# Kernel optimization log

Measured on AMD Instinct MI355X. Metric: run time of the kernel, lower is better.

Reference implementation:

```python
import jax, jax.numpy as jnp
import numpy as np

E = 64          # num_experts
DIM = 1024      # model dim
HID = 512       # per-expert FFN hidden dim
N = 65536       # total routed tokens (1024 per expert)


def setup_inputs() -> dict:
    key = jax.random.key(0)
    k_x, k1, k2, k3 = jax.random.split(key, 4)
    x = jax.random.normal(k_x, (N, DIM), dtype=jnp.float32)
    # learned params: w1/w3 [E, HID, DIM], w2 [E, DIM, HID] (trunc_normal std 0.02 ~ normal*0.02)
    w1 = jax.random.normal(k1, (E, HID, DIM), dtype=jnp.float32) * 0.02
    w2 = jax.random.normal(k2, (E, DIM, HID), dtype=jnp.float32) * 0.02
    w3 = jax.random.normal(k3, (E, HID, DIM), dtype=jnp.float32) * 0.02
    num_tokens_per_expert = jnp.full((E,), N // E, dtype=jnp.int32)
    return {"x": x, "w1": w1, "w2": w2, "w3": w3,
            "num_tokens_per_expert": num_tokens_per_expert}


def reference(x, w1, w2, w3, num_tokens_per_expert):
    # Grouped-GEMM SwiGLU expert FFN (torch._grouped_mm path, bf16 compute).
    bf16 = jnp.bfloat16
    xb = x.astype(bf16)                                   # [N, DIM]
    g = num_tokens_per_expert                             # [E] int32 group sizes
    w1t = jnp.swapaxes(w1.astype(bf16), 1, 2)             # [E, DIM, HID]
    w3t = jnp.swapaxes(w3.astype(bf16), 1, 2)             # [E, DIM, HID]
    w2t = jnp.swapaxes(w2.astype(bf16), 1, 2)             # [E, HID, DIM]
    h = jax.nn.silu(jax.lax.ragged_dot(xb, w1t, g))       # [N, HID]
    h = h * jax.lax.ragged_dot(xb, w3t, g)                # fused gate
    out = jax.lax.ragged_dot(h, w2t, g)                   # [N, DIM]
    return out.astype(x.dtype)
```

## Files before the change

kernel.cpp:

```cpp
#include <hip/hip_runtime.h>
#include <hip/hip_bf16.h>
#include <stdint.h>

#define NE   64
#define DIM  1024
#define HID  512
#define TPE  1024

typedef __attribute__((ext_vector_type(8)))  __bf16          bf16x8;
typedef __attribute__((ext_vector_type(4)))  float           f32x4;
typedef __attribute__((ext_vector_type(8)))  unsigned short  ushort8_t;
typedef __attribute__((ext_vector_type(4)))  float           float4_t;

__device__ __forceinline__ unsigned short f2bf(float f) {
  return __builtin_bit_cast(unsigned short, static_cast<__bf16>(f));
}
__device__ __forceinline__ float bf2f(unsigned short u) {
  unsigned int x = ((unsigned int)u) << 16;
  return __builtin_bit_cast(float, x);
}
__device__ __forceinline__ ushort8_t pack8(float4_t a, float4_t b) {
  ushort8_t r;
  r[0] = f2bf(a[0]); r[1] = f2bf(a[1]); r[2] = f2bf(a[2]); r[3] = f2bf(a[3]);
  r[4] = f2bf(b[0]); r[5] = f2bf(b[1]); r[6] = f2bf(b[2]); r[7] = f2bf(b[3]);
  return r;
}
__device__ __forceinline__ bf16x8 ldsfrag(const unsigned short* p) {
  return __builtin_bit_cast(bf16x8, *reinterpret_cast<const ushort8_t*>(p));
}

__device__ __forceinline__ void barrier_lgkm() {
  asm volatile("s_waitcnt lgkmcnt(0)" ::: "memory");
  __builtin_amdgcn_s_barrier();
}

#define LDK 40

__device__ __forceinline__ int xcd_swizzle(int bid, int nwg) {
  return (bid & 7) * (nwg >> 3) + (bid >> 3);
}

#define P1_NKT (DIM / 32)

__global__ __launch_bounds__(256, 2) void p1_kernel(
    const float* __restrict__ X, const float* __restrict__ W1,
    const float* __restrict__ W3, unsigned short* __restrict__ H) {
  __shared__ __align__(16) unsigned short lA [2][256 * LDK];
  __shared__ __align__(16) unsigned short lB1[2][ 64 * LDK];
  __shared__ __align__(16) unsigned short lB3[2][ 64 * LDK];

  const int tile = xcd_swizzle(blockIdx.x, NE * 4 * 8);
  const int e  = tile >> 5;
  const int tn = (tile >> 2) & 7;
  const int tm = tile & 3;
  const int t  = threadIdx.x;

  const float* gA  = X  + (size_t)(e * TPE + tm * 256) * DIM;
  const float* gB1 = W1 + ((size_t)e * HID + tn * 64) * DIM;
  const float* gB3 = W3 + ((size_t)e * HID + tn * 64) * DIM;

  const int ar = t >> 2, ac = (t & 3) * 8;

  float4_t a0[4][2], b10[2], b30[2];
  float4_t a1[4][2], b11[2], b31[2];

  auto load_g = [&](float4_t (&a)[4][2], float4_t (&b1)[2], float4_t (&b3)[2],
                    int kt) {
#pragma unroll
    for (int i = 0; i < 4; ++i) {
      const size_t o = (size_t)(ar + 64 * i) * DIM + kt * 32 + ac;
      a[i][0] = *reinterpret_cast<const float4_t*>(gA + o);
      a[i][1] = *reinterpret_cast<const float4_t*>(gA + o + 4);
    }
    const size_t ob = (size_t)ar * DIM + kt * 32 + ac;
    b1[0] = *reinterpret_cast<const float4_t*>(gB1 + ob);
    b1[1] = *reinterpret_cast<const float4_t*>(gB1 + ob + 4);
    b3[0] = *reinterpret_cast<const float4_t*>(gB3 + ob);
    b3[1] = *reinterpret_cast<const float4_t*>(gB3 + ob + 4);
  };
  auto store_l = [&](int buf, float4_t (&a)[4][2], float4_t (&b1)[2],
                     float4_t (&b3)[2]) {
#pragma unroll
    for (int i = 0; i < 4; ++i)
      *reinterpret_cast<ushort8_t*>(&lA[buf][(ar + 64 * i) * LDK + ac]) =
          pack8(a[i][0], a[i][1]);
    *reinterpret_cast<ushort8_t*>(&lB1[buf][ar * LDK + ac]) = pack8(b1[0], b1[1]);
    *reinterpret_cast<ushort8_t*>(&lB3[buf][ar * LDK + ac]) = pack8(b3[0], b3[1]);
  };

  const int lane = t & 63;
  const int wv   = t >> 6;
  const int wr   = wv >> 1, wc = wv & 1;
  const int fr   = lane & 15;
  const int ks   = (lane >> 4) * 8;

  f32x4 acc1[8][2], acc3[8][2];
#pragma unroll
  for (int m = 0; m < 8; ++m)
#pragma unroll
    for (int n = 0; n < 2; ++n)
#pragma unroll
      for (int i = 0; i < 4; ++i) { acc1[m][n][i] = 0.f; acc3[m][n][i] = 0.f; }

  auto mfma_phase = [&](int buf) {
    bf16x8 b1f[2], b3f[2];
#pragma unroll
    for (int n = 0; n < 2; ++n) {
      const int bi = (wc * 32 + n * 16 + fr) * LDK + ks;
      b1f[n] = ldsfrag(&lB1[buf][bi]);
      b3f[n] = ldsfrag(&lB3[buf][bi]);
    }
#pragma unroll
    for (int m = 0; m < 8; ++m) {
      const bf16x8 af = ldsfrag(&lA[buf][(wr * 128 + m * 16 + fr) * LDK + ks]);
#pragma unroll
      for (int n = 0; n < 2; ++n) {
        acc1[m][n] = __builtin_amdgcn_mfma_f32_16x16x32_bf16(af, b1f[n], acc1[m][n], 0, 0, 0);
        acc3[m][n] = __builtin_amdgcn_mfma_f32_16x16x32_bf16(af, b3f[n], acc3[m][n], 0, 0, 0);
      }
    }
  };

  load_g(a0, b10, b30, 0);
  load_g(a1, b11, b31, 1);
  for (int kt = 0; kt < P1_NKT; kt += 2) {
    store_l(0, a0, b10, b30);
    if (kt + 2 < P1_NKT) load_g(a0, b10, b30, kt + 2);
    barrier_lgkm();
    mfma_phase(0);
    store_l(1, a1, b11, b31);
    if (kt + 3 < P1_NKT) load_g(a1, b11, b31, kt + 3);
    barrier_lgkm();
    mfma_phase(1);
  }

  const int tokBase = e * TPE + tm * 256 + wr * 128 + (lane >> 4) * 4;
  const int hidBase = tn * 64 + wc * 32;
#pragma unroll
  for (int m = 0; m < 8; ++m)
#pragma unroll
    for (int n = 0; n < 2; ++n)
#pragma unroll
      for (int r = 0; r < 4; ++r) {
        const int tok = tokBase + m * 16 + r;
        const int hid = hidBase + n * 16 + fr;
        const float av = bf2f(f2bf(acc1[m][n][r]));
        const float bv = bf2f(f2bf(acc3[m][n][r]));
        const float s  = av / (1.0f + __expf(-av));
        H[(size_t)tok * HID + hid] = f2bf(s * bv);
      }
}

#define P2_NKT (HID / 32)

__global__ __launch_bounds__(256, 2) void p2_kernel(
    const unsigned short* __restrict__ Hin, const float* __restrict__ W2,
    float* __restrict__ OUT) {
  __shared__ __align__(16) unsigned short lA[2][256 * LDK];
  __shared__ __align__(16) unsigned short lB[2][128 * LDK];

  const int tile = xcd_swizzle(blockIdx.x, NE * 4 * 8);
  const int e  = tile >> 5;
  const int tn = (tile >> 2) & 7;
  const int tm = tile & 3;
  const int t  = threadIdx.x;

  const unsigned short* gA = Hin + (size_t)(e * TPE + tm * 256) * HID;
  const float*          gB = W2  + ((size_t)e * DIM + tn * 128) * HID;

  const int ar = t >> 2, ac = (t & 3) * 8;

  ushort8_t ha0[4], ha1[4];
  float4_t  wb0[2][2], wb1[2][2];

  auto load_g = [&](ushort8_t (&ha)[4], float4_t (&wb)[2][2], int kt) {
#pragma unroll
    for (int i = 0; i < 4; ++i)
      ha[i] = *reinterpret_cast<const ushort8_t*>(
          gA + (size_t)(ar + 64 * i) * HID + kt * 32 + ac);
#pragma unroll
    for (int i = 0; i < 2; ++i) {
      const size_t bo = (size_t)(ar + 64 * i) * HID + kt * 32 + ac;
      wb[i][0] = *reinterpret_cast<const float4_t*>(gB + bo);
      wb[i][1] = *reinterpret_cast<const float4_t*>(gB + bo + 4);
    }
  };
  auto store_l = [&](int buf, ushort8_t (&ha)[4], float4_t (&wb)[2][2]) {
#pragma unroll
    for (int i = 0; i < 4; ++i)
      *reinterpret_cast<ushort8_t*>(&lA[buf][(ar + 64 * i) * LDK + ac]) = ha[i];
#pragma unroll
    for (int i = 0; i < 2; ++i)
      *reinterpret_cast<ushort8_t*>(&lB[buf][(ar + 64 * i) * LDK + ac]) =
          pack8(wb[i][0], wb[i][1]);
  };

  const int lane = t & 63;
  const int wv   = t >> 6;
  const int wr   = wv >> 1, wc = wv & 1;
  const int fr   = lane & 15;
  const int ks   = (lane >> 4) * 8;

  f32x4 acc[8][4];
#pragma unroll
  for (int m = 0; m < 8; ++m)
#pragma unroll
    for (int n = 0; n < 4; ++n)
#pragma unroll
      for (int i = 0; i < 4; ++i) acc[m][n][i] = 0.f;

  auto mfma_phase = [&](int buf) {
    bf16x8 bfr[4];
#pragma unroll
    for (int n = 0; n < 4; ++n)
      bfr[n] = ldsfrag(&lB[buf][(wc * 64 + n * 16 + fr) * LDK + ks]);
#pragma unroll
    for (int m = 0; m < 8; ++m) {
      const bf16x8 af = ldsfrag(&lA[buf][(wr * 128 + m * 16 + fr) * LDK + ks]);
#pragma unroll
      for (int n = 0; n < 4; ++n)
        acc[m][n] = __builtin_amdgcn_mfma_f32_16x16x32_bf16(af, bfr[n], acc[m][n], 0, 0, 0);
    }
  };

  load_g(ha0, wb0, 0);
  load_g(ha1, wb1, 1);
  for (int kt = 0; kt < P2_NKT; kt += 2) {
    store_l(0, ha0, wb0);
    if (kt + 2 < P2_NKT) load_g(ha0, wb0, kt + 2);
    barrier_lgkm();
    mfma_phase(0);
    store_l(1, ha1, wb1);
    if (kt + 3 < P2_NKT) load_g(ha1, wb1, kt + 3);
    barrier_lgkm();
    mfma_phase(1);
  }

  const int tokBase = e * TPE + tm * 256 + wr * 128 + (lane >> 4) * 4;
  const int dBase   = tn * 128 + wc * 64;
#pragma unroll
  for (int m = 0; m < 8; ++m)
#pragma unroll
    for (int n = 0; n < 4; ++n)
#pragma unroll
      for (int r = 0; r < 4; ++r) {
        const int tok = tokBase + m * 16 + r;
        const int d   = dBase + n * 16 + fr;
        OUT[(size_t)tok * DIM + d] = bf2f(f2bf(acc[m][n][r]));
      }
}

extern "C" void kernel_launch(void* const* d_in, const int* in_sizes, int n_in,
                              void* d_out, int out_size, void* d_ws, size_t ws_size,
                              hipStream_t stream) {
  (void)in_sizes; (void)n_in; (void)out_size; (void)ws_size;
  const float* X  = (const float*)d_in[0];
  const float* W1 = (const float*)d_in[1];
  const float* W2 = (const float*)d_in[2];
  const float* W3 = (const float*)d_in[3];

  unsigned short* H = (unsigned short*)d_ws;
  float* OUT = (float*)d_out;

  p1_kernel<<<dim3(NE * 4 * 8), dim3(256), 0, stream>>>(X, W1, W3, H);
  p2_kernel<<<dim3(NE * 4 * 8), dim3(256), 0, stream>>>(H, W2, OUT);
}
```

Measured before the change: 517.5 us.

## Pre-convert weights to bf16 and rewrite GEMMs with direct global-to-LDS loads

Adds a weight-conversion kernel that casts W1/W3/W2 to bf16 once per call, interleaving W1 and W3 rows so one GEMM tile covers both gate and up projections. The two GEMM kernels are rewritten with 512-thread blocks, 256x256x64 tiles, XOR-swizzled LDS, and global_load_lds async copies for bf16 operands, with barriers and setprio placed around the MFMA blocks. The SwiGLU gate is combined through an LDS exchange between wave halves. This removes repeated fp32 weight loads and in-kernel conversion, at the cost of an extra pass over the weights and more workspace.

```diff
diff --git a/kernel.cpp b/kernel.cpp
--- a/kernel.cpp
+++ b/kernel.cpp
@@ -10,6 +10,7 @@
 typedef __attribute__((ext_vector_type(8)))  __bf16          bf16x8;
 typedef __attribute__((ext_vector_type(4)))  float           f32x4;
 typedef __attribute__((ext_vector_type(8)))  unsigned short  ushort8_t;
+typedef __attribute__((ext_vector_type(4)))  unsigned short  ushort4_t;
 typedef __attribute__((ext_vector_type(4)))  float           float4_t;
 
 __device__ __forceinline__ unsigned short f2bf(float f) {
@@ -28,226 +29,288 @@
 __device__ __forceinline__ bf16x8 ldsfrag(const unsigned short* p) {
   return __builtin_bit_cast(bf16x8, *reinterpret_cast<const ushort8_t*>(p));
 }
-
 __device__ __forceinline__ void barrier_lgkm() {
   asm volatile("s_waitcnt lgkmcnt(0)" ::: "memory");
   __builtin_amdgcn_s_barrier();
 }
-
-#define LDK 40
+typedef __attribute__((address_space(1))) const unsigned int gas_uint;
+typedef __attribute__((address_space(3))) unsigned int las_uint;
+__device__ __forceinline__ void gload16(const void* g, void* l) {
+  __builtin_amdgcn_global_load_lds((gas_uint*)g, (las_uint*)l, 16, 0, 0);
+}
 
 __device__ __forceinline__ int xcd_swizzle(int bid, int nwg) {
   return (bid & 7) * (nwg >> 3) + (bid >> 3);
 }
 
-#define P1_NKT (DIM / 32)
-
-__global__ __launch_bounds__(256, 2) void p1_kernel(
-    const float* __restrict__ X, const float* __restrict__ W1,
-    const float* __restrict__ W3, unsigned short* __restrict__ H) {
-  __shared__ __align__(16) unsigned short lA [2][256 * LDK];
-  __shared__ __align__(16) unsigned short lB1[2][ 64 * LDK];
-  __shared__ __align__(16) unsigned short lB3[2][ 64 * LDK];
-
-  const int tile = xcd_swizzle(blockIdx.x, NE * 4 * 8);
-  const int e  = tile >> 5;
-  const int tn = (tile >> 2) & 7;
+__global__ __launch_bounds__(256) void conv_w(
+    const float* __restrict__ W1, const float* __restrict__ W3,
+    const float* __restrict__ W2,
+    unsigned short* __restrict__ WB13, unsigned short* __restrict__ W2b) {
+  const int rb  = blockIdx.x;
+  const int reg = rb >> 9;
+  const int rbl = rb & 511;
+  const int f0  = rbl * 256 + threadIdx.x;
+  const int STRIDE = 512 * 256;
+
+  const float* src = (reg == 0) ? W1 : (reg == 1) ? W3 : W2;
+
+#pragma unroll 1
+  for (int it = 0; it < 8; ++it) {
+    float4_t v[4][2];
+    int f[4];
+#pragma unroll
+    for (int u = 0; u < 4; ++u) {
+      f[u] = f0 + (it * 4 + u) * STRIDE;
+      const float* p = src + (size_t)f[u] * 8;
+      v[u][0] = *reinterpret_cast<const float4_t*>(p);
+      v[u][1] = *reinterpret_cast<const float4_t*>(p + 4);
+    }
+#pragma unroll
+    for (int u = 0; u < 4; ++u) {
+      size_t dst;
+      if (reg == 2) {
+        dst = (size_t)f[u] * 8;
+        *reinterpret_cast<ushort8_t*>(W2b + dst) = pack8(v[u][0], v[u][1]);
+      } else {
+        const int e  = f[u] >> 16;
+        const int h  = (f[u] >> 7) & 511;
+        const int c8 = f[u] & 127;
+        const int g  = h >> 7, r = (h & 127) + (reg == 1 ? 128 : 0);
+        dst = ((((size_t)(e * 4 + g)) * 256 + r) * 128 + c8) * 8;
+        *reinterpret_cast<ushort8_t*>(WB13 + dst) = pack8(v[u][0], v[u][1]);
+      }
+    }
+  }
+}
+
+#define GEMM_IDS                                                               \
+  const int lane = threadIdx.x & 63;                                           \
+  const int wid  = threadIdx.x >> 6;                                           \
+  const int wr   = wid >> 2, wn = wid & 3;                                     \
+  const int fr   = lane & 15;                                                  \
+  const int c16b = lane >> 4;                                                  \
+  const int swz  = fr & 7;                                                     \
+  const int s_r  = lane >> 3;                                                  \
+  const int s_c  = ((lane & 7) ^ s_r) * 8;
+
+#define GEMM_ACC_INIT                                                          \
+  f32x4 acc[8][4];                                                             \
+  _Pragma("unroll") for (int m = 0; m < 8; ++m)                                \
+    _Pragma("unroll") for (int n = 0; n < 4; ++n)                              \
+      _Pragma("unroll") for (int i = 0; i < 4; ++i) acc[m][n][i] = 0.f;
+
+#define RD_FRAGS(buf, kk)                                                      \
+  bf16x8 af[8], bf0, bf1;                                                      \
+  (void)0
+
+__global__ __launch_bounds__(512, 2) void p1_fast(
+    const float* __restrict__ X, const unsigned short* __restrict__ WB13,
+    unsigned short* __restrict__ H) {
+  __shared__ __align__(16) unsigned short smem[2][2][256 * 64];
+
+  const int tile = xcd_swizzle(blockIdx.x, NE * 4 * 4);
+  const int e  = tile >> 4;
+  const int tm = (tile >> 2) & 3;
+  const int g  = tile & 3;
+  const float*          gA = X    + (size_t)(e * TPE + tm * 256) * DIM;
+  const unsigned short* gB = WB13 + (size_t)(e * 4 + g) * 256 * DIM;
+
+  GEMM_IDS
+  GEMM_ACC_INIT
+
+  const int arow = threadIdx.x >> 1, ah = threadIdx.x & 1;
+  float4_t fa[8];
+
+  auto loadA = [&](int kt) {
+    const float* p = gA + (size_t)arow * DIM + kt * 64 + ah * 32;
+#pragma unroll
+    for (int j = 0; j < 8; ++j)
+      fa[j] = *reinterpret_cast<const float4_t*>(p + j * 4);
+  };
+  auto writeA = [&](int buf) {
+    const int base = arow * 64;
+#pragma unroll
+    for (int j = 0; j < 4; ++j) {
+      const int gidx = (ah * 4 + j) ^ (arow & 7);
+      *reinterpret_cast<ushort8_t*>(&smem[buf][0][base + gidx * 8]) =
+          pack8(fa[2 * j], fa[2 * j + 1]);
+    }
+  };
+  auto stB = [&](int buf, int kt, int j) {
+    gload16(gB + (size_t)(j * 8 + s_r) * DIM + kt * 64 + s_c,
+            &smem[buf][1][j * 512]);
+  };
+  auto rdA = [&](int buf, int m, int kk) {
+    const int row = wr * 128 + m * 16 + fr;
+    return ldsfrag(&smem[buf][0][row * 64 + (((c16b + kk * 4) ^ swz) * 8)]);
+  };
+  auto rdB = [&](int buf, int nf, int kk) {
+    const int row = wn * 64 + nf * 16 + fr;
+    return ldsfrag(&smem[buf][1][row * 64 + (((c16b + kk * 4) ^ swz) * 8)]);
+  };
+
+  loadA(0);
+#pragma unroll 1
+  for (int j = 0; j < 4; ++j) stB(0, 0, wid * 4 + j);
+  writeA(0);
+
+  for (int kt = 0; kt < 16; ++kt) {
+    const int buf = kt & 1, sbuf = buf ^ 1;
+    const bool st = (kt + 1 < 16);
+    asm volatile("s_waitcnt vmcnt(0) lgkmcnt(0)" ::: "memory");
+    __builtin_amdgcn_s_barrier();
+    asm volatile("" ::: "memory");
+    if (st) loadA(kt + 1);
+    bf16x8 af[8];
+#pragma unroll
+    for (int q = 0; q < 4; ++q) {
+      const int kk = q >> 1, nh = q & 1;
+      if (nh == 0) {
+#pragma unroll
+        for (int m = 0; m < 8; ++m) af[m] = rdA(buf, m, kk);
+      }
+      bf16x8 bf0 = rdB(buf, nh * 2 + 0, kk);
+      bf16x8 bf1 = rdB(buf, nh * 2 + 1, kk);
+      if (st) stB(sbuf, kt + 1, wid * 4 + q);
+      asm volatile("" ::: "memory");
+      __builtin_amdgcn_s_barrier();
+      __builtin_amdgcn_s_setprio(1);
+#pragma unroll
+      for (int m = 0; m < 8; ++m) {
+        acc[m][nh * 2 + 0] = __builtin_amdgcn_mfma_f32_16x16x32_bf16(
+            af[m], bf0, acc[m][nh * 2 + 0], 0, 0, 0);
+        acc[m][nh * 2 + 1] = __builtin_amdgcn_mfma_f32_16x16x32_bf16(
+            af[m], bf1, acc[m][nh * 2 + 1], 0, 0, 0);
+      }
+      __builtin_amdgcn_s_setprio(0);
+    }
+    if (st) writeA(sbuf);
+  }
+
+  __builtin_amdgcn_s_barrier();
+  unsigned short* bex = &smem[0][0][0];
+  const int q4 = (lane >> 4) * 4;
+  if (wn >= 2) {
+#pragma unroll
+    for (int m = 0; m < 8; ++m)
+#pragma unroll
+      for (int n = 0; n < 4; ++n) {
+        const int hidl = (wn - 2) * 64 + n * 16 + fr;
+        const int tokl = wr * 128 + m * 16 + q4;
+        ushort4_t v;
+#pragma unroll
+        for (int r = 0; r < 4; ++r) v[r] = f2bf(acc[m][n][r]);
+        *reinterpret_cast<ushort4_t*>(&bex[hidl * 264 + tokl]) = v;
+      }
+  }
+  barrier_lgkm();
+  if (wn < 2) {
+    const int rowbase = e * TPE + tm * 256;
+#pragma unroll
+    for (int m = 0; m < 8; ++m)
+#pragma unroll
+      for (int n = 0; n < 4; ++n) {
+        const int hidl = wn * 64 + n * 16 + fr;
+        const int tokl = wr * 128 + m * 16 + q4;
+        const ushort4_t bv =
+            *reinterpret_cast<const ushort4_t*>(&bex[hidl * 264 + tokl]);
+#pragma unroll
+        for (int r = 0; r < 4; ++r) {
+          const float av = bf2f(f2bf(acc[m][n][r]));
+          const float b  = bf2f(bv[r]);
+          const float s  = av / (1.0f + __expf(-av));
+          H[(size_t)(rowbase + tokl + r) * HID + g * 128 + hidl] = f2bf(s * b);
+        }
+      }
+  }
+}
+
+__global__ __launch_bounds__(512, 2) void p2_fast(
+    const unsigned short* __restrict__ Hb, const unsigned short* __restrict__ W2b,
+    float* __restrict__ OUT) {
+  __shared__ __align__(16) unsigned short smem[2][2][256 * 64];
+
+  const int tile = xcd_swizzle(blockIdx.x, NE * 4 * 4);
+  const int e  = tile >> 4;
+  const int tn = (tile >> 2) & 3;
   const int tm = tile & 3;
-  const int t  = threadIdx.x;
-
-  const float* gA  = X  + (size_t)(e * TPE + tm * 256) * DIM;
-  const float* gB1 = W1 + ((size_t)e * HID + tn * 64) * DIM;
-  const float* gB3 = W3 + ((size_t)e * HID + tn * 64) * DIM;
-
-  const int ar = t >> 2, ac = (t & 3) * 8;
-
-  float4_t a0[4][2], b10[2], b30[2];
-  float4_t a1[4][2], b11[2], b31[2];
-
-  auto load_g = [&](float4_t (&a)[4][2], float4_t (&b1)[2], float4_t (&b3)[2],
-                    int kt) {
-#pragma unroll
-    for (int i = 0; i < 4; ++i) {
-      const size_t o = (size_t)(ar + 64 * i) * DIM + kt * 32 + ac;
-      a[i][0] = *reinterpret_cast<const float4_t*>(gA + o);
-      a[i][1] = *reinterpret_cast<const float4_t*>(gA + o + 4);
-    }
-    const size_t ob = (size_t)ar * DIM + kt * 32 + ac;
-    b1[0] = *reinterpret_cast<const float4_t*>(gB1 + ob);
-    b1[1] = *reinterpret_cast<const float4_t*>(gB1 + ob + 4);
-    b3[0] = *reinterpret_cast<const float4_t*>(gB3 + ob);
-    b3[1] = *reinterpret_cast<const float4_t*>(gB3 + ob + 4);
-  };
-  auto store_l = [&](int buf, float4_t (&a)[4][2], float4_t (&b1)[2],
-                     float4_t (&b3)[2]) {
-#pragma unroll
-    for (int i = 0; i < 4; ++i)
-      *reinterpret_cast<ushort8_t*>(&lA[buf][(ar + 64 * i) * LDK + ac]) =
-          pack8(a[i][0], a[i][1]);
-    *reinterpret_cast<ushort8_t*>(&lB1[buf][ar * LDK + ac]) = pack8(b1[0], b1[1]);
-    *reinterpret_cast<ushort8_t*>(&lB3[buf][ar * LDK + ac]) = pack8(b3[0], b3[1]);
-  };
-
-  const int lane = t & 63;
-  const int wv   = t >> 6;
-  const int wr   = wv >> 1, wc = wv & 1;
-  const int fr   = lane & 15;
-  const int ks   = (lane >> 4) * 8;
-
-  f32x4 acc1[8][2], acc3[8][2];
+  const unsigned short* gA = Hb  + (size_t)(e * TPE + tm * 256) * HID;
+  const unsigned short* gB = W2b + (size_t)(e * DIM + tn * 256) * HID;
+
+  GEMM_IDS
+  GEMM_ACC_INIT
+
+  auto stA = [&](int buf, int kt, int j) {
+    gload16(gA + (size_t)(j * 8 + s_r) * HID + kt * 64 + s_c,
+            &smem[buf][0][j * 512]);
+  };
+  auto stB = [&](int buf, int kt, int j) {
+    gload16(gB + (size_t)(j * 8 + s_r) * HID + kt * 64 + s_c,
+            &smem[buf][1][j * 512]);
+  };
+  auto rdA = [&](int buf, int m, int kk) {
+    const int row = wr * 128 + m * 16 + fr;
+    return ldsfrag(&smem[buf][0][row * 64 + (((c16b + kk * 4) ^ swz) * 8)]);
+  };
+  auto rdB = [&](int buf, int nf, int kk) {
+    const int row = wn * 64 + nf * 16 + fr;
+    return ldsfrag(&smem[buf][1][row * 64 + (((c16b + kk * 4) ^ swz) * 8)]);
+  };
+
+#pragma unroll 1
+  for (int j = 0; j < 4; ++j) stA(0, 0, wid * 4 + j);
+#pragma unroll 1
+  for (int j = 0; j < 4; ++j) stB(0, 0, wid * 4 + j);
+
+  for (int kt = 0; kt < 8; ++kt) {
+    const int buf = kt & 1, sbuf = buf ^ 1;
+    const bool st = (kt + 1 < 8);
+    asm volatile("s_waitcnt vmcnt(0) lgkmcnt(0)" ::: "memory");
+    __builtin_amdgcn_s_barrier();
+    asm volatile("" ::: "memory");
+    bf16x8 af[8];
+#pragma unroll
+    for (int q = 0; q < 4; ++q) {
+      const int kk = q >> 1, nh = q & 1;
+      if (nh == 0) {
+#pragma unroll
+        for (int m = 0; m < 8; ++m) af[m] = rdA(buf, m, kk);
+      }
+      bf16x8 bf0 = rdB(buf, nh * 2 + 0, kk);
+      bf16x8 bf1 = rdB(buf, nh * 2 + 1, kk);
+      if (st) {
+        if (q < 2) { stA(sbuf, kt + 1, wid * 4 + q * 2);
+                     stA(sbuf, kt + 1, wid * 4 + q * 2 + 1); }
+        else       { stB(sbuf, kt + 1, wid * 4 + (q - 2) * 2);
+                     stB(sbuf, kt + 1, wid * 4 + (q - 2) * 2 + 1); }
+      }
+      asm volatile("" ::: "memory");
+      __builtin_amdgcn_s_barrier();
+      __builtin_amdgcn_s_setprio(1);
+#pragma unroll
+      for (int m = 0; m < 8; ++m) {
+        acc[m][nh * 2 + 0] = __builtin_amdgcn_mfma_f32_16x16x32_bf16(
+            af[m], bf0, acc[m][nh * 2 + 0], 0, 0, 0);
+        acc[m][nh * 2 + 1] = __builtin_amdgcn_mfma_f32_16x16x32_bf16(
+            af[m], bf1, acc[m][nh * 2 + 1], 0, 0, 0);
+      }
+      __builtin_amdgcn_s_setprio(0);
+    }
+  }
+
+  const int q4 = (lane >> 4) * 4;
+  const int rowbase = e * TPE + tm * 256;
 #pragma unroll
   for (int m = 0; m < 8; ++m)
 #pragma unroll
-    for (int n = 0; n < 2; ++n)
-#pragma unroll
-      for (int i = 0; i < 4; ++i) { acc1[m][n][i] = 0.f; acc3[m][n][i] = 0.f; }
-
-  auto mfma_phase = [&](int buf) {
-    bf16x8 b1f[2], b3f[2];
-#pragma unroll
-    for (int n = 0; n < 2; ++n) {
-      const int bi = (wc * 32 + n * 16 + fr) * LDK + ks;
-      b1f[n] = ldsfrag(&lB1[buf][bi]);
-      b3f[n] = ldsfrag(&lB3[buf][bi]);
-    }
-#pragma unroll
-    for (int m = 0; m < 8; ++m) {
-      const bf16x8 af = ldsfrag(&lA[buf][(wr * 128 + m * 16 + fr) * LDK + ks]);
-#pragma unroll
-      for (int n = 0; n < 2; ++n) {
-        acc1[m][n] = __builtin_amdgcn_mfma_f32_16x16x32_bf16(af, b1f[n], acc1[m][n], 0, 0, 0);
-        acc3[m][n] = __builtin_amdgcn_mfma_f32_16x16x32_bf16(af, b3f[n], acc3[m][n], 0, 0, 0);
-      }
-    }
-  };
-
-  load_g(a0, b10, b30, 0);
-  load_g(a1, b11, b31, 1);
-  for (int kt = 0; kt < P1_NKT; kt += 2) {
-    store_l(0, a0, b10, b30);
-    if (kt + 2 < P1_NKT) load_g(a0, b10, b30, kt + 2);
-    barrier_lgkm();
-    mfma_phase(0);
-    store_l(1, a1, b11, b31);
-    if (kt + 3 < P1_NKT) load_g(a1, b11, b31, kt + 3);
-    barrier_lgkm();
-    mfma_phase(1);
-  }
-
-  const int tokBase = e * TPE + tm * 256 + wr * 128 + (lane >> 4) * 4;
-  const int hidBase = tn * 64 + wc * 32;
-#pragma unroll
-  for (int m = 0; m < 8; ++m)
-#pragma unroll
-    for (int n = 0; n < 2; ++n)
-#pragma unroll
-      for (int r = 0; r < 4; ++r) {
-        const int tok = tokBase + m * 16 + r;
-        const int hid = hidBase + n * 16 + fr;
-        const float av = bf2f(f2bf(acc1[m][n][r]));
-        const float bv = bf2f(f2bf(acc3[m][n][r]));
-        const float s  = av / (1.0f + __expf(-av));
-        H[(size_t)tok * HID + hid] = f2bf(s * bv);
-      }
-}
-
-#define P2_NKT (HID / 32)
-
-__global__ __launch_bounds__(256, 2) void p2_kernel(
-    const unsigned short* __restrict__ Hin, const float* __restrict__ W2,
-    float* __restrict__ OUT) {
-  __shared__ __align__(16) unsigned short lA[2][256 * LDK];
-  __shared__ __align__(16) unsigned short lB[2][128 * LDK];
-
-  const int tile = xcd_swizzle(blockIdx.x, NE * 4 * 8);
-  const int e  = tile >> 5;
-  const int tn = (tile >> 2) & 7;
-  const int tm = tile & 3;
-  const int t  = threadIdx.x;
-
-  const unsigned short* gA = Hin + (size_t)(e * TPE + tm * 256) * HID;
-  const float*          gB = W2  + ((size_t)e * DIM + tn * 128) * HID;
-
-  const int ar = t >> 2, ac = (t & 3) * 8;
-
-  ushort8_t ha0[4], ha1[4];
-  float4_t  wb0[2][2], wb1[2][2];
-
-  auto load_g = [&](ushort8_t (&ha)[4], float4_t (&wb)[2][2], int kt) {
-#pragma unroll
-    for (int i = 0; i < 4; ++i)
-      ha[i] = *reinterpret_cast<const ushort8_t*>(
-          gA + (size_t)(ar + 64 * i) * HID + kt * 32 + ac);
-#pragma unroll
-    for (int i = 0; i < 2; ++i) {
-      const size_t bo = (size_t)(ar + 64 * i) * HID + kt * 32 + ac;
-      wb[i][0] = *reinterpret_cast<const float4_t*>(gB + bo);
-      wb[i][1] = *reinterpret_cast<const float4_t*>(gB + bo + 4);
-    }
-  };
-  auto store_l = [&](int buf, ushort8_t (&ha)[4], float4_t (&wb)[2][2]) {
-#pragma unroll
-    for (int i = 0; i < 4; ++i)
-      *reinterpret_cast<ushort8_t*>(&lA[buf][(ar + 64 * i) * LDK + ac]) = ha[i];
-#pragma unroll
-    for (int i = 0; i < 2; ++i)
-      *reinterpret_cast<ushort8_t*>(&lB[buf][(ar + 64 * i) * LDK + ac]) =
-          pack8(wb[i][0], wb[i][1]);
-  };
-
-  const int lane = t & 63;
-  const int wv   = t >> 6;
-  const int wr   = wv >> 1, wc = wv & 1;
-  const int fr   = lane & 15;
-  const int ks   = (lane >> 4) * 8;
-
-  f32x4 acc[8][4];
-#pragma unroll
-  for (int m = 0; m < 8; ++m)
-#pragma unroll
-    for (int n = 0; n < 4; ++n)
-#pragma unroll
-      for (int i = 0; i < 4; ++i) acc[m][n][i] = 0.f;
-
-  auto mfma_phase = [&](int buf) {
-    bf16x8 bfr[4];
-#pragma unroll
-    for (int n = 0; n < 4; ++n)
-      bfr[n] = ldsfrag(&lB[buf][(wc * 64 + n * 16 + fr) * LDK + ks]);
-#pragma unroll
-    for (int m = 0; m < 8; ++m) {
-      const bf16x8 af = ldsfrag(&lA[buf][(wr * 128 + m * 16 + fr) * LDK + ks]);
-#pragma unroll
-      for (int n = 0; n < 4; ++n)
-        acc[m][n] = __builtin_amdgcn_mfma_f32_16x16x32_bf16(af, bfr[n], acc[m][n], 0, 0, 0);
-    }
-  };
-
-  load_g(ha0, wb0, 0);
-  load_g(ha1, wb1, 1);
-  for (int kt = 0; kt < P2_NKT; kt += 2) {
-    store_l(0, ha0, wb0);
-    if (kt + 2 < P2_NKT) load_g(ha0, wb0, kt + 2);
-    barrier_lgkm();
-    mfma_phase(0);
-    store_l(1, ha1, wb1);
-    if (kt + 3 < P2_NKT) load_g(ha1, wb1, kt + 3);
-    barrier_lgkm();
-    mfma_phase(1);
-  }
-
-  const int tokBase = e * TPE + tm * 256 + wr * 128 + (lane >> 4) * 4;
-  const int dBase   = tn * 128 + wc * 64;
-#pragma unroll
-  for (int m = 0; m < 8; ++m)
-#pragma unroll
-    for (int n = 0; n < 4; ++n)
-#pragma unroll
-      for (int r = 0; r < 4; ++r) {
-        const int tok = tokBase + m * 16 + r;
-        const int d   = dBase + n * 16 + fr;
-        OUT[(size_t)tok * DIM + d] = bf2f(f2bf(acc[m][n][r]));
-      }
+    for (int n = 0; n < 4; ++n) {
+      const int d    = tn * 256 + wn * 64 + n * 16 + fr;
+      const int tokl = wr * 128 + m * 16 + q4;
+#pragma unroll
+      for (int r = 0; r < 4; ++r)
+        OUT[(size_t)(rowbase + tokl + r) * DIM + d] = bf2f(f2bf(acc[m][n][r]));
+    }
 }
 
 extern "C" void kernel_launch(void* const* d_in, const int* in_sizes, int n_in,
@@ -258,10 +321,14 @@
   const float* W1 = (const float*)d_in[1];
   const float* W2 = (const float*)d_in[2];
   const float* W3 = (const float*)d_in[3];
-
-  unsigned short* H = (unsigned short*)d_ws;
   float* OUT = (float*)d_out;
 
-  p1_kernel<<<dim3(NE * 4 * 8), dim3(256), 0, stream>>>(X, W1, W3, H);
-  p2_kernel<<<dim3(NE * 4 * 8), dim3(256), 0, stream>>>(H, W2, OUT);
-}
+  const size_t MiB = 1024 * 1024;
+  unsigned short* WB13 = (unsigned short*)d_ws;
+  unsigned short* W2b  = WB13 + (size_t)128 * MiB / 2;
+  unsigned short* H    = WB13 + (size_t)192 * MiB / 2;
+
+  conv_w<<<dim3(1536), dim3(256), 0, stream>>>(W1, W3, W2, WB13, W2b);
+  p1_fast<<<dim3(NE * 4 * 4), dim3(512), 0, stream>>>(X, WB13, H);
+  p2_fast<<<dim3(NE * 4 * 4), dim3(512), 0, stream>>>(H, W2b, OUT);
+}
```

New measurement: 525.1 us. Within noise of the previous version (+1.5%).
